# Optimization experiments

Measured on AMD Instinct MI355X. Metric: run time of the kernel, lower is better.

The kernel has to match this reference:

```python
import jax, jax.numpy as jnp
import numpy as np

MAX_NUM_BINS = 200
BIN_SIZE = 500
NUM_NEIGHBORS = 5
DIST_MULT = 0.1


def setup_inputs() -> dict:
    key = jax.random.key(0)
    k1, k2 = jax.random.split(key)
    points = jax.random.normal(k1, (2, 5000, 128), dtype=jnp.float32)
    rotations = jax.random.normal(k2, (128, MAX_NUM_BINS // 2), dtype=jnp.float32)
    return {"points": points, "rotations": rotations}


def reference(points, rotations):
    # points: [B, N, D], rotations: [D, max_num_bins//2]
    B, N, D = points.shape
    nbins = N // BIN_SIZE  # module requires N % BIN_SIZE == 0

    # LSH bin assignment: project onto nbins//2 random directions, sign-split into nbins bins
    mul = jnp.einsum('bnd,dh->bnh', points, rotations[:, :nbins // 2])  # [B,N,nbins//2]
    cmul = jnp.concatenate([mul, -mul], axis=-1)                        # [B,N,nbins]
    bin_idx = jnp.argmax(cmul, axis=-1)                                 # [B,N]
    # equal-size bins via argsort of bin id (matches tf argsort+reshape)
    bins_split = jnp.argsort(bin_idx, axis=-1).reshape(B, nbins, BIN_SIZE)  # [B,nbins,S]

    # gather points per bin
    parts = jnp.take_along_axis(points, bins_split.reshape(B, N, 1), axis=1)
    parts = parts.reshape(B, nbins, BIN_SIZE, D)

    # per-bin pairwise distance -> gaussian kernel
    na = jnp.sum(parts * parts, axis=-1)                                # [B,nbins,S]
    gram = jnp.einsum('bcid,bcjd->bcij', parts, parts)                  # [B,nbins,S,S]
    dist = jnp.sqrt(jnp.maximum(na[..., :, None] - 2.0 * gram + na[..., None, :], 1e-6))
    dm = jnp.exp(-DIST_MULT * dist)                                     # [B,nbins,S,S]

    # top-k neighbors within each bin
    vals, idx = jax.lax.top_k(dm, NUM_NEIGHBORS)                        # [B,nbins,S,K]

    # map local bin indices back to global point indices
    bs_flat = bins_split.reshape(B * nbins, BIN_SIZE)
    dst = jnp.take_along_axis(bs_flat, idx.reshape(B * nbins, BIN_SIZE * NUM_NEIGHBORS), axis=1)
    dst = dst.reshape(B, nbins, BIN_SIZE, NUM_NEIGHBORS)
    src = jnp.broadcast_to(bins_split[..., None], dst.shape)
    bidx = jnp.broadcast_to(jnp.arange(B)[:, None, None, None], dst.shape)

    # scatter-add into dense [B,N,N] (sparse.add sums duplicate entries)
    out = jnp.zeros((B, N, N), dtype=points.dtype)
    out = out.at[bidx.reshape(-1), src.reshape(-1), dst.reshape(-1)].add(vals.reshape(-1))
    return out
```

## Files before the change

kernel.cpp:

```cpp
#include <hip/hip_runtime.h>
#include <cfloat>
#include <math.h>

#define NPTS   5000
#define BATCH  2
#define DIM    128
#define NBINS  10
#define BINSZ  500
#define TOPK   5
#define ROTCOLS 100

#define KB_PTS 64
#define KB_STR 129
__global__ void k_bins(const float* __restrict__ pts, const float* __restrict__ rot,
                       int* __restrict__ bin_idx, double* __restrict__ na) {
    __shared__ float P[KB_PTS * KB_STR];
    __shared__ float rotL[DIM * 5];
    int tid = threadIdx.x;
    for (int f = tid; f < DIM * 5; f += 256)
        rotL[f] = rot[(f / 5) * ROTCOLS + (f % 5)];

    int p0  = blockIdx.x * KB_PTS;
    int npb = min(KB_PTS, BATCH * NPTS - p0);

    for (int f = tid; f < npb * DIM; f += 256) {
        int r = f >> 7, d = f & 127;
        P[r * KB_STR + d] = pts[(size_t)(p0 + r) * DIM + d];
    }
    __syncthreads();

    int p = tid >> 2;
    int s = tid & 3;
    double acc[5] = {0., 0., 0., 0., 0.};
    double sq = 0.;
    const float* row = &P[p * KB_STR + s * 32];
    for (int j = 0; j < 32; ++j) {
        double v = (double)row[j];
        sq += v * v;
        int d = s * 32 + j;
#pragma unroll
        for (int h = 0; h < 5; ++h) acc[h] += v * (double)rotL[d * 5 + h];
    }
#pragma unroll
    for (int m = 1; m < 4; m <<= 1) {
#pragma unroll
        for (int h = 0; h < 5; ++h) acc[h] += __shfl_xor(acc[h], m, 4);
        sq += __shfl_xor(sq, m, 4);
    }
    if (s == 0 && p < npb) {
        double best = acc[0]; int bc = 0;
#pragma unroll
        for (int c = 1; c < NBINS; ++c) {
            double v = (c < 5) ? acc[c] : -acc[c - 5];
            if (v > best) { best = v; bc = c; }
        }
        bin_idx[p0 + p] = bc;
        na[p0 + p] = sq;
    }
}

__global__ void k_sort(const int* __restrict__ bin_idx, int* __restrict__ order) {
    const int b = blockIdx.x;
    const int t = threadIdx.x;
    const int NPT = (NPTS + 255) / 256;
    int start = t * NPT;
    int end   = min(NPTS, start + NPT);

    int cnt[NBINS];
#pragma unroll
    for (int c = 0; c < NBINS; ++c) cnt[c] = 0;
    for (int i = start; i < end; ++i) {
        int c = bin_idx[b * NPTS + i];
#pragma unroll
        for (int k = 0; k < NBINS; ++k) cnt[k] += (c == k);
    }

    __shared__ int hist[NBINS * 256];
#pragma unroll
    for (int c = 0; c < NBINS; ++c) hist[c * 256 + t] = cnt[c];
    __syncthreads();

    int base = t * NBINS;
    int s = 0;
#pragma unroll
    for (int k = 0; k < NBINS; ++k) s += hist[base + k];
    __shared__ int scan[256];
    scan[t] = s;
    __syncthreads();
    for (int off = 1; off < 256; off <<= 1) {
        int v = (t >= off) ? scan[t - off] : 0;
        __syncthreads();
        scan[t] += v;
        __syncthreads();
    }
    int run = scan[t] - s;
#pragma unroll
    for (int k = 0; k < NBINS; ++k) { int h = hist[base + k]; hist[base + k] = run; run += h; }
    __syncthreads();

    int ofs[NBINS];
#pragma unroll
    for (int c = 0; c < NBINS; ++c) ofs[c] = hist[c * 256 + t];
    for (int i = start; i < end; ++i) {
        int c = bin_idx[b * NPTS + i];
        int pos = 0;
#pragma unroll
        for (int k = 0; k < NBINS; ++k) {
            if (c == k) pos = ofs[k];
            ofs[k] += (c == k);
        }
        order[b * NPTS + pos] = i;
    }
}

#define RT    16
#define NRT   32
#define CTILE 64
#define RSTR  132
#define NCT   8
#define ROWQ  (NPTS/4)

__launch_bounds__(256, 3)
__global__ void k_chunks(const float* __restrict__ pts, const double* __restrict__ na,
                         const int* __restrict__ order, float* __restrict__ out) {
    __shared__ float  rowP[RT * RSTR];
    __shared__ float  colP[CTILE * RSTR];
    __shared__ double naC[CTILE];
    __shared__ double naRs[RT];
    __shared__ int    ordR[RT];

    int blk   = blockIdx.x;
    int rt    = blk & (NRT - 1);
    int chunk = blk >> 5;
    int b     = chunk / NBINS;
    int c     = chunk % NBINS;
    int tid   = threadIdx.x;
    int row0  = rt * RT;
    int rowCount = min(RT, BINSZ - row0);

    const int*   ordBase = order + b * NPTS + c * BINSZ;
    const float* ptsB    = pts + (size_t)b * NPTS * DIM;

    for (int f = tid; f < rowCount * (DIM / 4); f += 256) {
        int r = f / (DIM / 4);
        int q = f % (DIM / 4);
        int g = ordBase[row0 + r];
        float4 v = *(const float4*)(ptsB + (size_t)g * DIM + q * 4);
        *(float4*)(&rowP[r * RSTR + q * 4]) = v;
    }
    if (tid < rowCount) {
        int g = ordBase[row0 + tid];
        ordR[tid] = g;
        naRs[tid] = na[b * NPTS + g];
    }
    __syncthreads();

    int rg = tid >> 4;
    int cg = tid & 15;

    double naRr = (rg < rowCount) ? naRs[rg] : 0.;

    double tv[TOPK];
    int    tl[TOPK];
#pragma unroll
    for (int k = 0; k < TOPK; ++k) { tv[k] = DBL_MAX; tl[k] = 0x7fffffff; }

    const int totalZ = rowCount * ROWQ;

    for (int ct = 0; ct < NCT; ++ct) {
        int col0 = ct * CTILE;
        int colCount = min(CTILE, BINSZ - col0);
        __syncthreads();
        for (int f = tid; f < colCount * (DIM / 4); f += 256) {
            int j = f / (DIM / 4);
            int q = f % (DIM / 4);
            int g = ordBase[col0 + j];
            float4 v = *(const float4*)(ptsB + (size_t)g * DIM + q * 4);
            *(float4*)(&colP[j * RSTR + q * 4]) = v;
        }
        if (tid < colCount) {
            int g = ordBase[col0 + tid];
            naC[tid] = na[b * NPTS + g];
        }
        __syncthreads();

        {
            float4 z = make_float4(0.f, 0.f, 0.f, 0.f);
            int z0 = (ct * totalZ) / NCT, z1 = ((ct + 1) * totalZ) / NCT;
            for (int f = z0 + tid; f < z1; f += 256) {
                int r = f / ROWQ;
                int q = f - r * ROWQ;
                float* outRow = out + ((size_t)b * NPTS + ordR[r]) * NPTS;
                *(float4*)(outRow + 4 * q) = z;
            }
        }

        double acc[4];
#pragma unroll
        for (int jj = 0; jj < 4; ++jj) acc[jj] = 0.;

        const float4* rowP4 = (const float4*)(rowP);
        const float4* colP4 = (const float4*)(colP);
        for (int q = 0; q < DIM / 4; ++q) {
            float4 a = rowP4[rg * (RSTR / 4) + q];
            float4 bb[4];
#pragma unroll
            for (int jj = 0; jj < 4; ++jj) bb[jj] = colP4[(cg + 16 * jj) * (RSTR / 4) + q];
            double ad[4];
            ad[0] = (double)a.x; ad[1] = (double)a.y; ad[2] = (double)a.z; ad[3] = (double)a.w;
#pragma unroll
            for (int jj = 0; jj < 4; ++jj) {
                acc[jj] += ad[0] * (double)bb[jj].x + ad[1] * (double)bb[jj].y
                         + ad[2] * (double)bb[jj].z + ad[3] * (double)bb[jj].w;
            }
        }

#pragma unroll
        for (int jj = 0; jj < 4; ++jj) {
            int j = cg + 16 * jj;
            if (j < colCount) {
                int    cl = col0 + j;
                double cv = fmax(naRr + naC[j] - 2. * acc[jj], 1e-6);
#pragma unroll
                for (int k = 0; k < TOPK; ++k) {
                    bool lt = (cv < tv[k]);
                    double ov = tv[k]; int ol = tl[k];
                    if (lt) { tv[k] = cv; tl[k] = cl; cv = ov; cl = ol; }
                }
            }
        }
    }

#pragma unroll
    for (int m = 1; m < 16; m <<= 1) {
        double rv[TOPK]; int rl[TOPK];
#pragma unroll
        for (int k = 0; k < TOPK; ++k) {
            rv[k] = __shfl_xor(tv[k], m, 16);
            rl[k] = __shfl_xor(tl[k], m, 16);
        }
#pragma unroll
        for (int k = 0; k < TOPK; ++k) {
            double cv = rv[k]; int cl = rl[k];
#pragma unroll
            for (int s = 0; s < TOPK; ++s) {
                bool better = (cv < tv[s]) || (cv == tv[s] && cl < tl[s]);
                double ov = tv[s]; int ol = tl[s];
                if (better) { tv[s] = cv; tl[s] = cl; cv = ov; cl = ol; }
            }
        }
    }

    __syncthreads();

    if (cg == 0 && rg < rowCount) {
        int src = ordR[rg];
        float* outRow = out + ((size_t)b * NPTS + src) * NPTS;
#pragma unroll
        for (int k = 0; k < TOPK; ++k) {
            double dist = sqrt(tv[k]);
            double dm   = exp(-0.1 * dist);
            int dst = ordBase[tl[k]];
            outRow[dst] = (float)dm;
        }
    }
}

extern "C" void kernel_launch(void* const* d_in, const int* in_sizes, int n_in,
                              void* d_out, int out_size, void* d_ws, size_t ws_size,
                              hipStream_t stream) {
    const float* pts = (const float*)d_in[0];
    const float* rot = (const float*)d_in[1];
    float* out = (float*)d_out;

    double* na      = (double*)d_ws;
    int*    bin_idx = (int*)((char*)d_ws + (size_t)BATCH * NPTS * 8);
    int*    order   = (int*)((char*)d_ws + (size_t)BATCH * NPTS * 12);

    k_bins<<<(BATCH * NPTS + KB_PTS - 1) / KB_PTS, 256, 0, stream>>>(pts, rot, bin_idx, na);
    k_sort<<<BATCH, 256, 0, stream>>>(bin_idx, order);
    k_chunks<<<BATCH * NBINS * NRT, 256, 0, stream>>>(pts, na, order, out);
}
```

Measured before the change: 302.4 us.

## Use 2x2 register tile with pre-converted double row tile in chunk kernel

```diff
diff --git a/kernel.cpp b/kernel.cpp
--- a/kernel.cpp
+++ b/kernel.cpp
@@ -116,15 +116,16 @@
 #define RT    16
 #define NRT   32
 #define CTILE 64
-#define RSTR  132
+#define RSTRD 130
+#define CSTR  132
 #define NCT   8
 #define ROWQ  (NPTS/4)
 
 __launch_bounds__(256, 3)
 __global__ void k_chunks(const float* __restrict__ pts, const double* __restrict__ na,
                          const int* __restrict__ order, float* __restrict__ out) {
-    __shared__ float  rowP[RT * RSTR];
-    __shared__ float  colP[CTILE * RSTR];
+    __shared__ double rowPd[RT * RSTRD];
+    __shared__ float  colP[CTILE * CSTR];
     __shared__ double naC[CTILE];
     __shared__ double naRs[RT];
     __shared__ int    ordR[RT];
@@ -142,11 +143,14 @@
     const float* ptsB    = pts + (size_t)b * NPTS * DIM;
 
     for (int f = tid; f < rowCount * (DIM / 4); f += 256) {
-        int r = f / (DIM / 4);
-        int q = f % (DIM / 4);
+        int r = f >> 5;
+        int q = f & 31;
         int g = ordBase[row0 + r];
         float4 v = *(const float4*)(ptsB + (size_t)g * DIM + q * 4);
-        *(float4*)(&rowP[r * RSTR + q * 4]) = v;
+        double2 d01; d01.x = (double)v.x; d01.y = (double)v.y;
+        double2 d23; d23.x = (double)v.z; d23.y = (double)v.w;
+        *(double2*)(&rowPd[r * RSTRD + q * 4 + 0]) = d01;
+        *(double2*)(&rowPd[r * RSTRD + q * 4 + 2]) = d23;
     }
     if (tid < rowCount) {
         int g = ordBase[row0 + tid];
@@ -155,15 +159,18 @@
     }
     __syncthreads();
 
-    int rg = tid >> 4;
-    int cg = tid & 15;
-
-    double naRr = (rg < rowCount) ? naRs[rg] : 0.;
-
-    double tv[TOPK];
-    int    tl[TOPK];
-#pragma unroll
-    for (int k = 0; k < TOPK; ++k) { tv[k] = DBL_MAX; tl[k] = 0x7fffffff; }
+    int rg = tid >> 5;
+    int cg = tid & 31;
+
+    double naRr0 = (rg     < rowCount) ? naRs[rg]     : 0.;
+    double naRr1 = (rg + 8 < rowCount) ? naRs[rg + 8] : 0.;
+
+    double tv[2][TOPK];
+    int    tl[2][TOPK];
+#pragma unroll
+    for (int ii = 0; ii < 2; ++ii)
+#pragma unroll
+        for (int k = 0; k < TOPK; ++k) { tv[ii][k] = DBL_MAX; tl[ii][k] = 0x7fffffff; }
 
     const int totalZ = rowCount * ROWQ;
 
@@ -172,11 +179,11 @@
         int colCount = min(CTILE, BINSZ - col0);
         __syncthreads();
         for (int f = tid; f < colCount * (DIM / 4); f += 256) {
-            int j = f / (DIM / 4);
-            int q = f % (DIM / 4);
+            int j = f >> 5;
+            int q = f & 31;
             int g = ordBase[col0 + j];
             float4 v = *(const float4*)(ptsB + (size_t)g * DIM + q * 4);
-            *(float4*)(&colP[j * RSTR + q * 4]) = v;
+            *(float4*)(&colP[j * CSTR + q * 4]) = v;
         }
         if (tid < colCount) {
             int g = ordBase[col0 + tid];
@@ -195,73 +202,89 @@
             }
         }
 
-        double acc[4];
-#pragma unroll
-        for (int jj = 0; jj < 4; ++jj) acc[jj] = 0.;
-
-        const float4* rowP4 = (const float4*)(rowP);
-        const float4* colP4 = (const float4*)(colP);
+        double acc00 = 0., acc01 = 0., acc10 = 0., acc11 = 0.;
+
         for (int q = 0; q < DIM / 4; ++q) {
-            float4 a = rowP4[rg * (RSTR / 4) + q];
-            float4 bb[4];
-#pragma unroll
-            for (int jj = 0; jj < 4; ++jj) bb[jj] = colP4[(cg + 16 * jj) * (RSTR / 4) + q];
-            double ad[4];
-            ad[0] = (double)a.x; ad[1] = (double)a.y; ad[2] = (double)a.z; ad[3] = (double)a.w;
-#pragma unroll
-            for (int jj = 0; jj < 4; ++jj) {
-                acc[jj] += ad[0] * (double)bb[jj].x + ad[1] * (double)bb[jj].y
-                         + ad[2] * (double)bb[jj].z + ad[3] * (double)bb[jj].w;
-            }
-        }
-
-#pragma unroll
-        for (int jj = 0; jj < 4; ++jj) {
-            int j = cg + 16 * jj;
+            double2 a0lo = *(const double2*)(&rowPd[rg * RSTRD + q * 4 + 0]);
+            double2 a0hi = *(const double2*)(&rowPd[rg * RSTRD + q * 4 + 2]);
+            double2 a1lo = *(const double2*)(&rowPd[(rg + 8) * RSTRD + q * 4 + 0]);
+            double2 a1hi = *(const double2*)(&rowPd[(rg + 8) * RSTRD + q * 4 + 2]);
+            float4 b0 = *(const float4*)(&colP[cg * CSTR + q * 4]);
+            float4 b1 = *(const float4*)(&colP[(cg + 32) * CSTR + q * 4]);
+            double b00 = (double)b0.x, b01 = (double)b0.y,
+                   b02 = (double)b0.z, b03 = (double)b0.w;
+            double b10 = (double)b1.x, b11 = (double)b1.y,
+                   b12 = (double)b1.z, b13 = (double)b1.w;
+            acc00 += a0lo.x * b00 + a0lo.y * b01 + a0hi.x * b02 + a0hi.y * b03;
+            acc01 += a0lo.x * b10 + a0lo.y * b11 + a0hi.x * b12 + a0hi.y * b13;
+            acc10 += a1lo.x * b00 + a1lo.y * b01 + a1hi.x * b02 + a1hi.y * b03;
+            acc11 += a1lo.x * b10 + a1lo.y * b11 + a1hi.x * b12 + a1hi.y * b13;
+        }
+
+#pragma unroll
+        for (int jj = 0; jj < 2; ++jj) {
+            int j = cg + 32 * jj;
             if (j < colCount) {
                 int    cl = col0 + j;
-                double cv = fmax(naRr + naC[j] - 2. * acc[jj], 1e-6);
+                double nc = naC[j];
+                double a0 = (jj == 0) ? acc00 : acc01;
+                double a1 = (jj == 0) ? acc10 : acc11;
+                double cv0 = fmax(naRr0 + nc - 2. * a0, 1e-6);
+                double cv1 = fmax(naRr1 + nc - 2. * a1, 1e-6);
+                int cl0 = cl, cl1 = cl;
 #pragma unroll
                 for (int k = 0; k < TOPK; ++k) {
-                    bool lt = (cv < tv[k]);
-                    double ov = tv[k]; int ol = tl[k];
-                    if (lt) { tv[k] = cv; tl[k] = cl; cv = ov; cl = ol; }
+                    bool lt0 = (cv0 < tv[0][k]);
+                    double ov0 = tv[0][k]; int ol0 = tl[0][k];
+                    if (lt0) { tv[0][k] = cv0; tl[0][k] = cl0; cv0 = ov0; cl0 = ol0; }
+                    bool lt1 = (cv1 < tv[1][k]);
+                    double ov1 = tv[1][k]; int ol1 = tl[1][k];
+                    if (lt1) { tv[1][k] = cv1; tl[1][k] = cl1; cv1 = ov1; cl1 = ol1; }
                 }
             }
         }
     }
 
 #pragma unroll
-    for (int m = 1; m < 16; m <<= 1) {
-        double rv[TOPK]; int rl[TOPK];
-#pragma unroll
-        for (int k = 0; k < TOPK; ++k) {
-            rv[k] = __shfl_xor(tv[k], m, 16);
-            rl[k] = __shfl_xor(tl[k], m, 16);
-        }
-#pragma unroll
-        for (int k = 0; k < TOPK; ++k) {
-            double cv = rv[k]; int cl = rl[k];
-#pragma unroll
-            for (int s = 0; s < TOPK; ++s) {
-                bool better = (cv < tv[s]) || (cv == tv[s] && cl < tl[s]);
-                double ov = tv[s]; int ol = tl[s];
-                if (better) { tv[s] = cv; tl[s] = cl; cv = ov; cl = ol; }
-            }
-        }
-    }
-
-    __syncthreads();
-
-    if (cg == 0 && rg < rowCount) {
-        int src = ordR[rg];
-        float* outRow = out + ((size_t)b * NPTS + src) * NPTS;
-#pragma unroll
-        for (int k = 0; k < TOPK; ++k) {
-            double dist = sqrt(tv[k]);
-            double dm   = exp(-0.1 * dist);
-            int dst = ordBase[tl[k]];
-            outRow[dst] = (float)dm;
+    for (int m = 1; m < 32; m <<= 1) {
+#pragma unroll
+        for (int ii = 0; ii < 2; ++ii) {
+            double rv[TOPK]; int rl[TOPK];
+#pragma unroll
+            for (int k = 0; k < TOPK; ++k) {
+                rv[k] = __shfl_xor(tv[ii][k], m, 32);
+                rl[k] = __shfl_xor(tl[ii][k], m, 32);
+            }
+#pragma unroll
+            for (int k = 0; k < TOPK; ++k) {
+                double cv = rv[k]; int cl = rl[k];
+#pragma unroll
+                for (int s = 0; s < TOPK; ++s) {
+                    bool better = (cv < tv[ii][s]) || (cv == tv[ii][s] && cl < tl[ii][s]);
+                    double ov = tv[ii][s]; int ol = tl[ii][s];
+                    if (better) { tv[ii][s] = cv; tl[ii][s] = cl; cv = ov; cl = ol; }
+                }
+            }
+        }
+    }
+
+    __syncthreads();
+
+    if (cg == 0) {
+#pragma unroll
+        for (int ii = 0; ii < 2; ++ii) {
+            int r = rg + 8 * ii;
+            if (r < rowCount) {
+                int src = ordR[r];
+                float* outRow = out + ((size_t)b * NPTS + src) * NPTS;
+#pragma unroll
+                for (int k = 0; k < TOPK; ++k) {
+                    double dist = sqrt(tv[ii][k]);
+                    double dm   = exp(-0.1 * dist);
+                    int dst = ordBase[tl[ii][k]];
+                    outRow[dst] = (float)dm;
+                }
+            }
         }
     }
 }
@@ -274,8 +297,8 @@
     float* out = (float*)d_out;
 
     double* na      = (double*)d_ws;
-    int*    bin_idx = (int*)((char*)d_ws + (size_t)BATCH * NPTS * 8);
-    int*    order   = (int*)((char*)d_ws + (size_t)BATCH * NPTS * 12);
+    int*    bin_idx = (int*)((char*)d_ws + 80000);
+    int*    order   = (int*)((char*)d_ws + 120000);
 
     k_bins<<<(BATCH * NPTS + KB_PTS - 1) / KB_PTS, 256, 0, stream>>>(pts, rot, bin_idx, na);
     k_sort<<<BATCH, 256, 0, stream>>>(bin_idx, order);
```

Result: faster. 296.3 us (median of 3 runs) (-2.0%).
